# Performance work log

Hardware: AMD Instinct MI355X
Metric: run time of the kernel (lower is better)

Reference implementation:

```python
import jax, jax.numpy as jnp
import numpy as np

NV, NE, NH, NI = 50000, 10000, 512, 300000

def setup_inputs() -> dict:
    key = jax.random.key(0)
    ks = jax.random.split(key, 12)
    v = jax.random.normal(ks[0], (NV, NH), dtype=jnp.float32)
    e = jax.random.normal(ks[1], (NE, NH), dtype=jnp.float32)
    player_idx = jax.random.randint(ks[2], (NI,), 0, NV)
    game_idx = jax.random.randint(ks[3], (NI,), 0, NE)
    idx = jnp.arange(NI)
    W_v2e = jax.random.normal(ks[4], (NH, NH), dtype=jnp.float32)
    W_e2v = jax.random.normal(ks[5], (NH, NH), dtype=jnp.float32)
    b_v = jnp.zeros((NH,), dtype=jnp.float32)
    b_e = jnp.zeros((NH,), dtype=jnp.float32)
    v_weight = jax.random.uniform(ks[6], (NV, 1), dtype=jnp.float32) * 0.5 + 0.5
    e_weight = jax.random.uniform(ks[7], (NE, 1), dtype=jnp.float32) * 0.5 + 0.5
    v_reg_weight = jax.random.uniform(ks[8], (NI, 1), dtype=jnp.float32) * 0.5 + 0.5
    e_reg_weight = jax.random.uniform(ks[9], (NI, 1), dtype=jnp.float32) * 0.5 + 0.5
    e_reg_sum = jax.random.uniform(ks[10], (NE, 1), dtype=jnp.float32) + 1.0
    v_reg_sum = jax.random.uniform(ks[11], (NV, 1), dtype=jnp.float32) + 1.0
    return {"v": v, "e": e, "player_idx": player_idx, "game_idx": game_idx, "idx": idx,
            "W_v2e": W_v2e, "W_e2v": W_e2v, "b_v": b_v, "b_e": b_e,
            "v_weight": v_weight, "e_weight": e_weight,
            "v_reg_weight": v_reg_weight, "e_reg_weight": e_reg_weight,
            "v_reg_sum": v_reg_sum, "e_reg_sum": e_reg_sum}

def reference(v, e, player_idx, game_idx, idx, W_v2e, W_e2v, b_v, b_e,
              v_weight, e_weight, v_reg_weight, e_reg_weight, v_reg_sum, e_reg_sum):
    # vertex -> edge message (edge_linear=False branch: ReLU)
    ve = jax.nn.relu(v @ W_v2e + b_v)                    # [nv, nh]
    v_out = v * v_weight                                  # v_fac = 1 (predict_edge=False)
    ve_g = (ve * v_weight)[player_idx] * v_reg_weight[idx]  # [ni, nh] gather + per-incidence reg
    e_out = e + jax.ops.segment_sum(ve_g, game_idx, num_segments=NE)
    e_out = e_out / e_reg_sum
    # edge -> vertex message
    ev = jax.nn.relu(e_out @ W_e2v + b_e)                 # [ne, nh]
    ev_g = (ev * e_weight)[game_idx] * e_reg_weight[idx]  # [ni, nh]
    v_out = v_out + jax.ops.segment_sum(ev_g, player_idx, num_segments=NV)
    v_out = v_out / v_reg_sum
    # dropout_p = 0 -> identity; is_last=False, use_edge_lin=False
    return (v_out, e_out)
```

## Files before the change

kernel.cpp:

```cpp
#include <hip/hip_runtime.h>

#define NV 50000
#define NE 10000
#define NH 512
#define NI_TOT 300000
#define PB 40000

typedef __attribute__((ext_vector_type(8))) short short8v;
typedef __attribute__((ext_vector_type(4))) float f32x4;
typedef __attribute__((ext_vector_type(4))) unsigned short ushort4v;

__device__ __forceinline__ unsigned short f2bf(float x) {
    union { float f; unsigned int u; } v; v.f = x;
    unsigned int r = (v.u + 0x7FFFu + ((v.u >> 16) & 1u)) >> 16;
    return (unsigned short)r;
}
__device__ __forceinline__ unsigned int pack2bf(float lo, float hi) {
    return (unsigned int)f2bf(lo) | ((unsigned int)f2bf(hi) << 16);
}
__device__ __forceinline__ float bf2f(unsigned short u) {
    union { unsigned int x; float f; } v; v.x = ((unsigned int)u) << 16;
    return v.f;
}

__global__ __launch_bounds__(256) void cast_f32_bf16(
    const float* __restrict__ src, unsigned short* __restrict__ dst, int n8)
{
    const int i = blockIdx.x * 256 + threadIdx.x;
    if (i >= n8) return;
    const float4 a = reinterpret_cast<const float4*>(src)[2 * i];
    const float4 b = reinterpret_cast<const float4*>(src)[2 * i + 1];
    uint4 o;
    o.x = pack2bf(a.x, a.y); o.y = pack2bf(a.z, a.w);
    o.z = pack2bf(b.x, b.y); o.w = pack2bf(b.z, b.w);
    reinterpret_cast<uint4*>(dst)[i] = o;
}

__global__ __launch_bounds__(256) void gemm_mfma_bf16a_bf16out(
    const unsigned short* __restrict__ Abf, const unsigned short* __restrict__ Bt,
    const float* __restrict__ bias, const float* __restrict__ rowscale,
    unsigned short* __restrict__ Cbf, int M)
{
    __shared__ unsigned short As[128][72];
    __shared__ unsigned short Bs[128][72];

    const int tid  = threadIdx.x;
    const int lane = tid & 63;
    const int wave = tid >> 6;
    const int wm   = (wave & 1) * 64;
    const int wn   = (wave >> 1) * 64;
    const int tileM = blockIdx.y * 128;
    const int col0  = blockIdx.x * 128;

    f32x4 acc[4][4] = {};
    const short8v zero8 = {0, 0, 0, 0, 0, 0, 0, 0};

    for (int k0 = 0; k0 < NH; k0 += 64) {
        #pragma unroll
        for (int j = 0; j < 4; ++j) {
            const int chunk = j * 256 + tid;
            const int n  = chunk >> 3;
            const int kc = (chunk & 7) * 8;
            const int arow = tileM + n;
            short8v a = zero8;
            if (arow < M)
                a = *reinterpret_cast<const short8v*>(&Abf[(size_t)arow * NH + k0 + kc]);
            *reinterpret_cast<short8v*>(&As[n][kc]) = a;
        }
        #pragma unroll
        for (int j = 0; j < 4; ++j) {
            const int chunk = j * 256 + tid;
            const int n  = chunk >> 3;
            const int kc = (chunk & 7) * 8;
            short8v b = *reinterpret_cast<const short8v*>(
                &Bt[(size_t)(col0 + n) * NH + k0 + kc]);
            *reinterpret_cast<short8v*>(&Bs[n][kc]) = b;
        }
        __syncthreads();

        #pragma unroll
        for (int ks = 0; ks < 2; ++ks) {
            const int koff = ks * 32 + (lane >> 4) * 8;
            short8v af[4], bfr[4];
            #pragma unroll
            for (int mf = 0; mf < 4; ++mf)
                af[mf] = *reinterpret_cast<short8v*>(&As[wm + mf * 16 + (lane & 15)][koff]);
            #pragma unroll
            for (int nf = 0; nf < 4; ++nf)
                bfr[nf] = *reinterpret_cast<short8v*>(&Bs[wn + nf * 16 + (lane & 15)][koff]);
            #pragma unroll
            for (int mf = 0; mf < 4; ++mf)
                #pragma unroll
                for (int nf = 0; nf < 4; ++nf)
                    acc[mf][nf] = __builtin_amdgcn_mfma_f32_16x16x32_bf16(
                        af[mf], bfr[nf], acc[mf][nf], 0, 0, 0);
        }
        __syncthreads();
    }

    const int rgrp = (lane >> 4) * 4;
    const int cin  = lane & 15;
    #pragma unroll
    for (int mf = 0; mf < 4; ++mf) {
        #pragma unroll
        for (int r = 0; r < 4; ++r) {
            const int row = tileM + wm + mf * 16 + rgrp + r;
            if (row < M) {
                const float rs = rowscale[row];
                #pragma unroll
                for (int nf = 0; nf < 4; ++nf) {
                    const int col = col0 + wn + nf * 16 + cin;
                    Cbf[(size_t)row * NH + col] =
                        f2bf(fmaxf(acc[mf][nf][r] + bias[col], 0.f) * rs);
                }
            }
        }
    }
}

__global__ __launch_bounds__(256) void gemm_mfma_bf16a(
    const unsigned short* __restrict__ Abf, const unsigned short* __restrict__ Bt,
    const float* __restrict__ bias, const float* __restrict__ rowscale,
    float* __restrict__ C, int M)
{
    __shared__ unsigned short As[128][72];
    __shared__ unsigned short Bs[128][72];

    const int tid  = threadIdx.x;
    const int lane = tid & 63;
    const int wave = tid >> 6;
    const int wm   = (wave & 1) * 64;
    const int wn   = (wave >> 1) * 64;
    const int tileM = blockIdx.y * 128;
    const int col0  = blockIdx.x * 128;

    f32x4 acc[4][4] = {};
    const short8v zero8 = {0, 0, 0, 0, 0, 0, 0, 0};

    for (int k0 = 0; k0 < NH; k0 += 64) {
        #pragma unroll
        for (int j = 0; j < 4; ++j) {
            const int chunk = j * 256 + tid;
            const int n  = chunk >> 3;
            const int kc = (chunk & 7) * 8;
            const int arow = tileM + n;
            short8v a = zero8;
            if (arow < M)
                a = *reinterpret_cast<const short8v*>(&Abf[(size_t)arow * NH + k0 + kc]);
            *reinterpret_cast<short8v*>(&As[n][kc]) = a;
        }
        #pragma unroll
        for (int j = 0; j < 4; ++j) {
            const int chunk = j * 256 + tid;
            const int n  = chunk >> 3;
            const int kc = (chunk & 7) * 8;
            short8v b = *reinterpret_cast<const short8v*>(
                &Bt[(size_t)(col0 + n) * NH + k0 + kc]);
            *reinterpret_cast<short8v*>(&Bs[n][kc]) = b;
        }
        __syncthreads();

        #pragma unroll
        for (int ks = 0; ks < 2; ++ks) {
            const int koff = ks * 32 + (lane >> 4) * 8;
            short8v af[4], bfr[4];
            #pragma unroll
            for (int mf = 0; mf < 4; ++mf)
                af[mf] = *reinterpret_cast<short8v*>(&As[wm + mf * 16 + (lane & 15)][koff]);
            #pragma unroll
            for (int nf = 0; nf < 4; ++nf)
                bfr[nf] = *reinterpret_cast<short8v*>(&Bs[wn + nf * 16 + (lane & 15)][koff]);
            #pragma unroll
            for (int mf = 0; mf < 4; ++mf)
                #pragma unroll
                for (int nf = 0; nf < 4; ++nf)
                    acc[mf][nf] = __builtin_amdgcn_mfma_f32_16x16x32_bf16(
                        af[mf], bfr[nf], acc[mf][nf], 0, 0, 0);
        }
        __syncthreads();
    }

    const int rgrp = (lane >> 4) * 4;
    const int cin  = lane & 15;
    #pragma unroll
    for (int mf = 0; mf < 4; ++mf) {
        #pragma unroll
        for (int r = 0; r < 4; ++r) {
            const int row = tileM + wm + mf * 16 + rgrp + r;
            if (row < M) {
                const float rs = rowscale[row];
                #pragma unroll
                for (int nf = 0; nf < 4; ++nf) {
                    const int col = col0 + wn + nf * 16 + cin;
                    C[(size_t)row * NH + col] = fmaxf(acc[mf][nf][r] + bias[col], 0.f) * rs;
                }
            }
        }
    }
}

__global__ __launch_bounds__(256) void gemm_mfma_relu_scale(
    const float* __restrict__ A, const unsigned short* __restrict__ Bt,
    const float* __restrict__ bias, const float* __restrict__ rowscale,
    float* __restrict__ C, int M)
{
    __shared__ unsigned short As[128][72];
    __shared__ unsigned short Bs[128][72];

    const int tid  = threadIdx.x;
    const int lane = tid & 63;
    const int wave = tid >> 6;
    const int wm   = (wave & 1) * 64;
    const int wn   = (wave >> 1) * 64;
    const int tileM = blockIdx.y * 128;
    const int col0  = blockIdx.x * 128;

    f32x4 acc[4][4] = {};

    for (int k0 = 0; k0 < NH; k0 += 64) {
        #pragma unroll
        for (int j = 0; j < 8; ++j) {
            const int r = j * 16 + (tid >> 4);
            const int c = (tid & 15) * 4;
            const int arow = tileM + r;
            float4 av = make_float4(0.f, 0.f, 0.f, 0.f);
            if (arow < M)
                av = *reinterpret_cast<const float4*>(&A[(size_t)arow * NH + k0 + c]);
            unsigned short* dst = &As[r][c];
            dst[0] = f2bf(av.x); dst[1] = f2bf(av.y);
            dst[2] = f2bf(av.z); dst[3] = f2bf(av.w);
        }
        #pragma unroll
        for (int j = 0; j < 4; ++j) {
            const int chunk = j * 256 + tid;
            const int n  = chunk >> 3;
            const int kc = (chunk & 7) * 8;
            short8v b = *reinterpret_cast<const short8v*>(
                &Bt[(size_t)(col0 + n) * NH + k0 + kc]);
            *reinterpret_cast<short8v*>(&Bs[n][kc]) = b;
        }
        __syncthreads();

        #pragma unroll
        for (int ks = 0; ks < 2; ++ks) {
            const int koff = ks * 32 + (lane >> 4) * 8;
            short8v af[4], bfr[4];
            #pragma unroll
            for (int mf = 0; mf < 4; ++mf)
                af[mf] = *reinterpret_cast<short8v*>(&As[wm + mf * 16 + (lane & 15)][koff]);
            #pragma unroll
            for (int nf = 0; nf < 4; ++nf)
                bfr[nf] = *reinterpret_cast<short8v*>(&Bs[wn + nf * 16 + (lane & 15)][koff]);
            #pragma unroll
            for (int mf = 0; mf < 4; ++mf)
                #pragma unroll
                for (int nf = 0; nf < 4; ++nf)
                    acc[mf][nf] = __builtin_amdgcn_mfma_f32_16x16x32_bf16(
                        af[mf], bfr[nf], acc[mf][nf], 0, 0, 0);
        }
        __syncthreads();
    }

    const int rgrp = (lane >> 4) * 4;
    const int cin  = lane & 15;
    #pragma unroll
    for (int mf = 0; mf < 4; ++mf) {
        #pragma unroll
        for (int r = 0; r < 4; ++r) {
            const int row = tileM + wm + mf * 16 + rgrp + r;
            if (row < M) {
                const float rs = rowscale[row];
                #pragma unroll
                for (int nf = 0; nf < 4; ++nf) {
                    const int col = col0 + wn + nf * 16 + cin;
                    C[(size_t)row * NH + col] = fmaxf(acc[mf][nf][r] + bias[col], 0.f) * rs;
                }
            }
        }
    }
}

__global__ __launch_bounds__(256) void transpose_cast_w(
    const float* __restrict__ W, unsigned short* __restrict__ Wt)
{
    __shared__ float t[32][33];
    const int bx = blockIdx.x;
    const int by = blockIdx.y;
    const int tx = threadIdx.x & 31;
    const int ty = threadIdx.x >> 5;
    #pragma unroll
    for (int j = 0; j < 32; j += 8)
        t[ty + j][tx] = W[(size_t)(by * 32 + ty + j) * NH + bx * 32 + tx];
    __syncthreads();
    #pragma unroll
    for (int j = 0; j < 32; j += 8)
        Wt[(size_t)(bx * 32 + ty + j) * NH + by * 32 + tx] = f2bf(t[tx][ty + j]);
}

__global__ __launch_bounds__(256) void gemm_relu_scale(
    const float* __restrict__ A, const float* __restrict__ B,
    const float* __restrict__ bias, const float* __restrict__ rowscale,
    float* __restrict__ C, int M)
{
    __shared__ float As[16][68];
    __shared__ float Bs[16][64];
    const int tid = threadIdx.x;
    const int tx = tid & 15;
    const int ty = tid >> 4;
    const int tileM = blockIdx.y * 64;
    const int col0  = blockIdx.x * 64;
    const int lr  = tid >> 2;
    const int lk4 = (tid & 3) * 4;
    const int bc  = tid & 63;
    const int bk  = tid >> 6;
    float acc[4][4] = {};
    for (int k0 = 0; k0 < NH; k0 += 16) {
        const int arow = tileM + lr;
        float4 av = make_float4(0.f, 0.f, 0.f, 0.f);
        if (arow < M)
            av = *reinterpret_cast<const float4*>(&A[(size_t)arow * NH + k0 + lk4]);
        As[lk4 + 0][lr] = av.x; As[lk4 + 1][lr] = av.y;
        As[lk4 + 2][lr] = av.z; As[lk4 + 3][lr] = av.w;
        #pragma unroll
        for (int jj = 0; jj < 4; ++jj) {
            const int kk = bk + jj * 4;
            Bs[kk][bc] = B[(size_t)(k0 + kk) * NH + col0 + bc];
        }
        __syncthreads();
        #pragma unroll
        for (int kk = 0; kk < 16; ++kk) {
            float4 a = *reinterpret_cast<const float4*>(&As[kk][ty * 4]);
            float4 b = *reinterpret_cast<const float4*>(&Bs[kk][tx * 4]);
            acc[0][0] += a.x * b.x; acc[0][1] += a.x * b.y; acc[0][2] += a.x * b.z; acc[0][3] += a.x * b.w;
            acc[1][0] += a.y * b.x; acc[1][1] += a.y * b.y; acc[1][2] += a.y * b.z; acc[1][3] += a.y * b.w;
            acc[2][0] += a.z * b.x; acc[2][1] += a.z * b.y; acc[2][2] += a.z * b.z; acc[2][3] += a.z * b.w;
            acc[3][0] += a.w * b.x; acc[3][1] += a.w * b.y; acc[3][2] += a.w * b.z; acc[3][3] += a.w * b.w;
        }
        __syncthreads();
    }
    const int rbase = tileM + ty * 4;
    const int cbase = col0 + tx * 4;
    #pragma unroll
    for (int i = 0; i < 4; ++i) {
        const int row = rbase + i;
        if (row < M) {
            const float s = rowscale[row];
            float4 o;
            o.x = fmaxf(acc[i][0] + bias[cbase + 0], 0.f) * s;
            o.y = fmaxf(acc[i][1] + bias[cbase + 1], 0.f) * s;
            o.z = fmaxf(acc[i][2] + bias[cbase + 2], 0.f) * s;
            o.w = fmaxf(acc[i][3] + bias[cbase + 3], 0.f) * s;
            *reinterpret_cast<float4*>(&C[(size_t)row * NH + cbase]) = o;
        }
    }
}

__global__ __launch_bounds__(256) void zero_ints(int* __restrict__ p, int n)
{
    const int i = blockIdx.x * 256 + threadIdx.x;
    if (i < n) p[i] = 0;
}

__global__ __launch_bounds__(256) void hist_kernel(
    const int* __restrict__ gi, const int* __restrict__ pi,
    int* __restrict__ e_cnt, int* __restrict__ v_cnt)
{
    const int i = blockIdx.x * 256 + threadIdx.x;
    if (i >= NI_TOT) return;
    atomicAdd(&e_cnt[gi[i]], 1);
    atomicAdd(&v_cnt[pi[i]], 1);
}

__global__ __launch_bounds__(256) void scan_local(
    const int* __restrict__ cnt, int* __restrict__ off, int* __restrict__ bsum, int n)
{
    __shared__ int buf[256];
    const int t = threadIdx.x;
    const int gi = blockIdx.x * 256 + t;
    int x = (gi < n) ? cnt[gi] : 0;
    buf[t] = x;
    __syncthreads();
    #pragma unroll
    for (int d = 1; d < 256; d <<= 1) {
        int y = (t >= d) ? buf[t - d] : 0;
        __syncthreads();
        buf[t] += y;
        __syncthreads();
    }
    if (gi < n) off[gi + 1] = buf[t];
    if (t == 255) bsum[blockIdx.x] = buf[255];
}

__global__ __launch_bounds__(256) void scan_bsums(int* __restrict__ bsum, int nb)
{
    __shared__ int buf[256];
    const int t = threadIdx.x;
    const int x = (t < nb) ? bsum[t] : 0;
    buf[t] = x;
    __syncthreads();
    #pragma unroll
    for (int d = 1; d < 256; d <<= 1) {
        int y = (t >= d) ? buf[t - d] : 0;
        __syncthreads();
        buf[t] += y;
        __syncthreads();
    }
    if (t < nb) bsum[t] = buf[t] - x;
}

__global__ __launch_bounds__(256) void scan_add(
    int* __restrict__ off, const int* __restrict__ bsum, int n)
{
    const int gi = blockIdx.x * 256 + threadIdx.x;
    if (gi == 0) off[0] = 0;
    if (gi < n) off[gi + 1] += bsum[blockIdx.x];
}

__global__ __launch_bounds__(256) void scan_kernel(
    const int* __restrict__ cnt, int* __restrict__ off, int n)
{
    __shared__ int buf[256];
    __shared__ int carry_s;
    const int t = threadIdx.x;
    if (t == 0) { off[0] = 0; carry_s = 0; }
    __syncthreads();
    for (int base = 0; base < n; base += 256) {
        int x = (base + t < n) ? cnt[base + t] : 0;
        buf[t] = x;
        __syncthreads();
        #pragma unroll
        for (int d = 1; d < 256; d <<= 1) {
            int y = (t >= d) ? buf[t - d] : 0;
            __syncthreads();
            buf[t] += y;
            __syncthreads();
        }
        if (base + t < n) off[base + t + 1] = buf[t] + carry_s;
        __syncthreads();
        if (t == 255) carry_s += buf[255];
        __syncthreads();
    }
}

__global__ __launch_bounds__(256) void fill_kernel(
    const int* __restrict__ gi, const int* __restrict__ pi,
    const int* __restrict__ e_off, int* __restrict__ e_cur, int* __restrict__ e_list,
    const int* __restrict__ v_off, int* __restrict__ v_cur, int* __restrict__ v_list)
{
    const int i = blockIdx.x * 256 + threadIdx.x;
    if (i >= NI_TOT) return;
    const int g = gi[i];
    e_list[e_off[g] + atomicAdd(&e_cur[g], 1)] = i;
    const int p = pi[i];
    v_list[v_off[p] + atomicAdd(&v_cur[p], 1)] = i;
}

__global__ __launch_bounds__(128) void agg_e_bf16(
    const float* __restrict__ e, const unsigned short* __restrict__ ve_bf,
    const int* __restrict__ player_idx, const float* __restrict__ v_reg_weight,
    const int* __restrict__ e_off, const int* __restrict__ e_list,
    const float* __restrict__ e_reg_sum, float* __restrict__ out_e,
    unsigned short* __restrict__ Ebf)
{
    __shared__ int   sp[128];
    __shared__ float sw[128];
    const int g = blockIdx.x;
    const int t = threadIdx.x;
    const int c = t << 2;
    float4 acc = *reinterpret_cast<const float4*>(&e[(size_t)g * NH + c]);
    const int beg = e_off[g], end = e_off[g + 1];
    for (int base = beg; base < end; base += 128) {
        const int m = min(128, end - base);
        __syncthreads();
        if (t < m) {
            const int i = e_list[base + t];
            sp[t] = player_idx[i];
            sw[t] = v_reg_weight[i];
        }
        __syncthreads();
        #pragma unroll 4
        for (int j = 0; j < m; ++j) {
            const int   p = sp[j];
            const float w = sw[j];
            ushort4v x = *reinterpret_cast<const ushort4v*>(&ve_bf[(size_t)p * NH + c]);
            acc.x += w * bf2f(x.x); acc.y += w * bf2f(x.y);
            acc.z += w * bf2f(x.z); acc.w += w * bf2f(x.w);
        }
    }
    const float inv = 1.0f / e_reg_sum[g];
    acc.x *= inv; acc.y *= inv; acc.z *= inv; acc.w *= inv;
    *reinterpret_cast<float4*>(&out_e[(size_t)g * NH + c]) = acc;
    uint2 pk;
    pk.x = pack2bf(acc.x, acc.y);
    pk.y = pack2bf(acc.z, acc.w);
    *reinterpret_cast<uint2*>(&Ebf[(size_t)g * NH + c]) = pk;
}

__global__ __launch_bounds__(128) void agg_v_bf16(
    const float* __restrict__ v, const float* __restrict__ v_weight,
    const unsigned short* __restrict__ ev_bf,
    const int* __restrict__ game_idx, const float* __restrict__ e_reg_weight,
    const int* __restrict__ v_off, const int* __restrict__ v_list,
    const float* __restrict__ v_reg_sum, float* __restrict__ out_v)
{
    __shared__ int   sg[128];
    __shared__ float sw[128];
    const int p = blockIdx.x;
    const int t = threadIdx.x;
    const int c = t << 2;
    const float vw = v_weight[p];
    float4 acc = *reinterpret_cast<const float4*>(&v[(size_t)p * NH + c]);
    acc.x *= vw; acc.y *= vw; acc.z *= vw; acc.w *= vw;
    const int beg = v_off[p], end = v_off[p + 1];
    for (int base = beg; base < end; base += 128) {
        const int m = min(128, end - base);
        __syncthreads();
        if (t < m) {
            const int i = v_list[base + t];
            sg[t] = game_idx[i];
            sw[t] = e_reg_weight[i];
        }
        __syncthreads();
        #pragma unroll 4
        for (int j = 0; j < m; ++j) {
            const int   g = sg[j];
            const float w = sw[j];
            ushort4v x = *reinterpret_cast<const ushort4v*>(&ev_bf[(size_t)g * NH + c]);
            acc.x += w * bf2f(x.x); acc.y += w * bf2f(x.y);
            acc.z += w * bf2f(x.z); acc.w += w * bf2f(x.w);
        }
    }
    const float inv = 1.0f / v_reg_sum[p];
    acc.x *= inv; acc.y *= inv; acc.z *= inv; acc.w *= inv;
    *reinterpret_cast<float4*>(&out_v[(size_t)p * NH + c]) = acc;
}

__global__ __launch_bounds__(128) void agg_e_kernel(
    const float* __restrict__ e, const float* __restrict__ ve_w,
    const int* __restrict__ player_idx, const float* __restrict__ v_reg_weight,
    const int* __restrict__ e_off, const int* __restrict__ e_list,
    const float* __restrict__ e_reg_sum, float* __restrict__ out_e)
{
    __shared__ int   sp[128];
    __shared__ float sw[128];
    const int g = blockIdx.x;
    const int t = threadIdx.x;
    const int c = t << 2;
    float4 acc = *reinterpret_cast<const float4*>(&e[(size_t)g * NH + c]);
    const int beg = e_off[g], end = e_off[g + 1];
    for (int base = beg; base < end; base += 128) {
        const int m = min(128, end - base);
        __syncthreads();
        if (t < m) {
            const int i = e_list[base + t];
            sp[t] = player_idx[i];
            sw[t] = v_reg_weight[i];
        }
        __syncthreads();
        #pragma unroll 4
        for (int j = 0; j < m; ++j) {
            const int   p = sp[j];
            const float w = sw[j];
            float4 x = *reinterpret_cast<const float4*>(&ve_w[(size_t)p * NH + c]);
            acc.x += w * x.x; acc.y += w * x.y; acc.z += w * x.z; acc.w += w * x.w;
        }
    }
    const float inv = 1.0f / e_reg_sum[g];
    acc.x *= inv; acc.y *= inv; acc.z *= inv; acc.w *= inv;
    *reinterpret_cast<float4*>(&out_e[(size_t)g * NH + c]) = acc;
}

__global__ __launch_bounds__(128) void agg_v_kernel(
    const float* __restrict__ v, const float* __restrict__ v_weight,
    const float* __restrict__ ev_w,
    const int* __restrict__ game_idx, const float* __restrict__ e_reg_weight,
    const int* __restrict__ v_off, const int* __restrict__ v_list,
    const float* __restrict__ v_reg_sum, float* __restrict__ out_v)
{
    __shared__ int   sg[128];
    __shared__ float sw[128];
    const int p = blockIdx.x;
    const int t = threadIdx.x;
    const int c = t << 2;
    const float vw = v_weight[p];
    float4 acc = *reinterpret_cast<const float4*>(&v[(size_t)p * NH + c]);
    acc.x *= vw; acc.y *= vw; acc.z *= vw; acc.w *= vw;
    const int beg = v_off[p], end = v_off[p + 1];
    for (int base = beg; base < end; base += 128) {
        const int m = min(128, end - base);
        __syncthreads();
        if (t < m) {
            const int i = v_list[base + t];
            sg[t] = game_idx[i];
            sw[t] = e_reg_weight[i];
        }
        __syncthreads();
        #pragma unroll 4
        for (int j = 0; j < m; ++j) {
            const int   g = sg[j];
            const float w = sw[j];
            float4 x = *reinterpret_cast<const float4*>(&ev_w[(size_t)g * NH + c]);
            acc.x += w * x.x; acc.y += w * x.y; acc.z += w * x.z; acc.w += w * x.w;
        }
    }
    const float inv = 1.0f / v_reg_sum[p];
    acc.x *= inv; acc.y *= inv; acc.z *= inv; acc.w *= inv;
    *reinterpret_cast<float4*>(&out_v[(size_t)p * NH + c]) = acc;
}

__global__ __launch_bounds__(256) void scatter_add_kernel(
    const float* __restrict__ src, const int* __restrict__ gidx,
    const int* __restrict__ sidx, const float* __restrict__ regw,
    float* __restrict__ dst, int ni, int smin, int smax, int gmax)
{
    const int i = blockIdx.x * 2 + (threadIdx.x >> 7);
    if (i >= ni) return;
    const int s = sidx[i];
    if (s < smin || s >= smax) return;
    const int g = gidx[i];
    if (g < 0 || g >= gmax) return;
    const int c = (threadIdx.x & 127) << 2;
    const float w = regw[i];
    float4 val = *reinterpret_cast<const float4*>(&src[(size_t)g * NH + c]);
    float* d = &dst[(size_t)s * NH + c];
    atomicAdd(d + 0, val.x * w);
    atomicAdd(d + 1, val.y * w);
    atomicAdd(d + 2, val.z * w);
    atomicAdd(d + 3, val.w * w);
}

__global__ __launch_bounds__(256) void recompute_ev_scatter(
    const float* __restrict__ e_out, const float* __restrict__ W,
    const float* __restrict__ bias, const float* __restrict__ e_weight,
    const int* __restrict__ player_idx, const int* __restrict__ game_idx,
    const float* __restrict__ e_reg_weight, float* __restrict__ out_v, int pmin)
{
    const int i = blockIdx.x;
    const int p = player_idx[i];
    if (p < pmin || p >= NV) return;
    const int g = game_idx[i];
    if (g < 0 || g >= NE) return;
    __shared__ float eg[NH];
    const int t = threadIdx.x;
    eg[t]       = e_out[(size_t)g * NH + t];
    eg[t + 256] = e_out[(size_t)g * NH + t + 256];
    __syncthreads();
    float s0 = 0.f, s1 = 0.f;
    #pragma unroll 4
    for (int k = 0; k < NH; ++k) {
        const float ek = eg[k];
        s0 += ek * W[(size_t)k * NH + t];
        s1 += ek * W[(size_t)k * NH + t + 256];
    }
    const float ew = e_weight[g] * e_reg_weight[i];
    atomicAdd(&out_v[(size_t)p * NH + t],       fmaxf(s0 + bias[t], 0.f) * ew);
    atomicAdd(&out_v[(size_t)p * NH + t + 256], fmaxf(s1 + bias[t + 256], 0.f) * ew);
}

__global__ __launch_bounds__(256) void init_copy(
    const float* __restrict__ src, float* __restrict__ dst, int n4)
{
    const int i = blockIdx.x * 256 + threadIdx.x;
    if (i < n4)
        reinterpret_cast<float4*>(dst)[i] = reinterpret_cast<const float4*>(src)[i];
}

__global__ __launch_bounds__(256) void init_scale_rows(
    const float* __restrict__ src, const float* __restrict__ w,
    float* __restrict__ dst, int n4)
{
    const int i = blockIdx.x * 256 + threadIdx.x;
    if (i >= n4) return;
    const int row = i >> 7;
    const float s = w[row];
    float4 v = reinterpret_cast<const float4*>(src)[i];
    v.x *= s; v.y *= s; v.z *= s; v.w *= s;
    reinterpret_cast<float4*>(dst)[i] = v;
}

__global__ __launch_bounds__(256) void div_rows(
    const float* __restrict__ rs, float* __restrict__ x, int n4)
{
    const int i = blockIdx.x * 256 + threadIdx.x;
    if (i >= n4) return;
    const int row = i >> 7;
    const float inv = 1.0f / rs[row];
    float4 v = reinterpret_cast<float4*>(x)[i];
    v.x *= inv; v.y *= inv; v.z *= inv; v.w *= inv;
    reinterpret_cast<float4*>(x)[i] = v;
}

extern "C" void kernel_launch(void* const* d_in, const int* in_sizes, int n_in,
                              void* d_out, int out_size, void* d_ws, size_t ws_size,
                              hipStream_t stream) {
    const float* v            = (const float*)d_in[0];
    const float* e            = (const float*)d_in[1];
    const int*   player_idx   = (const int*)d_in[2];
    const int*   game_idx     = (const int*)d_in[3];
    const float* W_v2e        = (const float*)d_in[5];
    const float* W_e2v        = (const float*)d_in[6];
    const float* b_v          = (const float*)d_in[7];
    const float* b_e          = (const float*)d_in[8];

    const float* a9  = (const float*)d_in[9];
    const float* a10 = (const float*)d_in[10];
    const float* v_weight = (in_sizes[9]  == NV) ? a9  : a10;
    const float* e_weight = (in_sizes[9]  == NV) ? a10 : a9;
    const float* v_reg_weight = (const float*)d_in[11];
    const float* e_reg_weight = (const float*)d_in[12];
    const float* a13 = (const float*)d_in[13];
    const float* a14 = (const float*)d_in[14];
    const float* e_reg_sum = (in_sizes[13] == NE) ? a13 : a14;
    const float* v_reg_sum = (in_sizes[13] == NE) ? a14 : a13;

    float* out_v = (float*)d_out;
    float* out_e = (float*)d_out + (size_t)NV * NH;

    const dim3 blk(256);
    const int NB_E = (NE + 255) / 256;
    const int NB_V = (NV + 255) / 256;

    float* ev_w = (float*)d_ws;
    int* e_cnt  = (int*)((char*)d_ws + (size_t)NE * NH * sizeof(float));
    int* v_cnt  = e_cnt + NE;
    int* e_cur  = v_cnt + NV;
    int* v_cur  = e_cur + NE;
    int* e_off  = v_cur + NV;
    int* v_off  = e_off + NE + 1;
    int* e_list = v_off + NV + 1;
    int* v_list = e_list + NI_TOT;
    int* e_bsum = v_list + NI_TOT;
    int* v_bsum = e_bsum + NB_E;
    unsigned short* Wt1 = (unsigned short*)(v_bsum + NB_V);
    unsigned short* Wt2 = Wt1 + (size_t)NH * NH;
    unsigned short* Abf = Wt2 + (size_t)NH * NH;
    unsigned short* Ebf = Abf + (size_t)NV * NH;
    const size_t csr_need  = (size_t)((char*)(v_list + NI_TOT) - (char*)d_ws);
    const size_t mfma_need = (size_t)((char*)(Abf)            - (char*)d_ws);
    const size_t bf16_need = (size_t)((char*)(Ebf + (size_t)NE * NH) - (char*)d_ws);

    if (ws_size >= mfma_need && d_ws != nullptr) {
        const bool bf16a = (ws_size >= bf16_need);
        transpose_cast_w<<<dim3(16, 16), blk, 0, stream>>>(W_v2e, Wt1);
        transpose_cast_w<<<dim3(16, 16), blk, 0, stream>>>(W_e2v, Wt2);
        if (bf16a)
            cast_f32_bf16<<<(NV * NH / 8 + 255) / 256, blk, 0, stream>>>(
                v, Abf, NV * NH / 8);
        const int nz = 2 * (NE + NV);
        zero_ints<<<(nz + 255) / 256, blk, 0, stream>>>(e_cnt, nz);
        hist_kernel<<<(NI_TOT + 255) / 256, blk, 0, stream>>>(
            game_idx, player_idx, e_cnt, v_cnt);
        scan_local<<<NB_E, blk, 0, stream>>>(e_cnt, e_off, e_bsum, NE);
        scan_bsums<<<1, blk, 0, stream>>>(e_bsum, NB_E);
        scan_add<<<NB_E, blk, 0, stream>>>(e_off, e_bsum, NE);
        scan_local<<<NB_V, blk, 0, stream>>>(v_cnt, v_off, v_bsum, NV);
        scan_bsums<<<1, blk, 0, stream>>>(v_bsum, NB_V);
        scan_add<<<NB_V, blk, 0, stream>>>(v_off, v_bsum, NV);
        fill_kernel<<<(NI_TOT + 255) / 256, blk, 0, stream>>>(
            game_idx, player_idx, e_off, e_cur, e_list, v_off, v_cur, v_list);

        if (bf16a) {
            unsigned short* ve_bf = (unsigned short*)out_v;
            gemm_mfma_bf16a_bf16out<<<dim3(NH / 128, (NV + 127) / 128), blk, 0, stream>>>(
                Abf, Wt1, b_v, v_weight, ve_bf, NV);
            agg_e_bf16<<<NE, dim3(128), 0, stream>>>(
                e, ve_bf, player_idx, v_reg_weight, e_off, e_list, e_reg_sum,
                out_e, Ebf);
            unsigned short* ev_bf = (unsigned short*)ev_w;
            gemm_mfma_bf16a_bf16out<<<dim3(NH / 128, (NE + 127) / 128), blk, 0, stream>>>(
                Ebf, Wt2, b_e, e_weight, ev_bf, NE);
            agg_v_bf16<<<NV, dim3(128), 0, stream>>>(
                v, v_weight, ev_bf, game_idx, e_reg_weight, v_off, v_list,
                v_reg_sum, out_v);
        } else {
            gemm_mfma_relu_scale<<<dim3(NH / 128, (NV + 127) / 128), blk, 0, stream>>>(
                v, Wt1, b_v, v_weight, out_v, NV);
            agg_e_kernel<<<NE, dim3(128), 0, stream>>>(
                e, out_v, player_idx, v_reg_weight, e_off, e_list, e_reg_sum, out_e);
            gemm_mfma_relu_scale<<<dim3(NH / 128, (NE + 127) / 128), blk, 0, stream>>>(
                out_e, Wt2, b_e, e_weight, ev_w, NE);
            agg_v_kernel<<<NV, dim3(128), 0, stream>>>(
                v, v_weight, ev_w, game_idx, e_reg_weight, v_off, v_list,
                v_reg_sum, out_v);
        }
        return;
    }

    if (ws_size >= csr_need && d_ws != nullptr) {
        gemm_relu_scale<<<dim3(NH / 64, (NV + 63) / 64), blk, 0, stream>>>(
            v, W_v2e, b_v, v_weight, out_v, NV);
        const int nz = 2 * (NE + NV);
        zero_ints<<<(nz + 255) / 256, blk, 0, stream>>>(e_cnt, nz);
        hist_kernel<<<(NI_TOT + 255) / 256, blk, 0, stream>>>(
            game_idx, player_idx, e_cnt, v_cnt);
        scan_kernel<<<1, blk, 0, stream>>>(e_cnt, e_off, NE);
        scan_kernel<<<1, blk, 0, stream>>>(v_cnt, v_off, NV);
        fill_kernel<<<(NI_TOT + 255) / 256, blk, 0, stream>>>(
            game_idx, player_idx, e_off, e_cur, e_list, v_off, v_cur, v_list);
        agg_e_kernel<<<NE, dim3(128), 0, stream>>>(
            e, out_v, player_idx, v_reg_weight, e_off, e_list, e_reg_sum, out_e);
        gemm_relu_scale<<<dim3(NH / 64, (NE + 63) / 64), blk, 0, stream>>>(
            out_e, W_e2v, b_e, e_weight, ev_w, NE);
        agg_v_kernel<<<NV, dim3(128), 0, stream>>>(
            v, v_weight, ev_w, game_idx, e_reg_weight, v_off, v_list,
            v_reg_sum, out_v);
        return;
    }

    const size_t evw_bytes = (size_t)NE * NH * sizeof(float);
    const bool big_ws = (ws_size >= evw_bytes) && (d_ws != nullptr);
    float* ev_w2 = big_ws ? (float*)d_ws : (out_v + (size_t)PB * NH);
    const int pb = big_ws ? NV : PB;
    const int n4_e = NE * NH / 4;

    gemm_relu_scale<<<dim3(NH / 64, (NV + 63) / 64), blk, 0, stream>>>(
        v, W_v2e, b_v, v_weight, out_v, NV);
    init_copy<<<(n4_e + 255) / 256, blk, 0, stream>>>(e, out_e, n4_e);
    scatter_add_kernel<<<(NI_TOT + 1) / 2, blk, 0, stream>>>(
        out_v, player_idx, game_idx, v_reg_weight, out_e, NI_TOT, 0, NE, NV);
    div_rows<<<(n4_e + 255) / 256, blk, 0, stream>>>(e_reg_sum, out_e, n4_e);
    gemm_relu_scale<<<dim3(NH / 64, (NE + 63) / 64), blk, 0, stream>>>(
        out_e, W_e2v, b_e, e_weight, ev_w2, NE);
    {
        const int n4 = pb * NH / 4;
        init_scale_rows<<<(n4 + 255) / 256, blk, 0, stream>>>(v, v_weight, out_v, n4);
    }
    scatter_add_kernel<<<(NI_TOT + 1) / 2, blk, 0, stream>>>(
        ev_w2, game_idx, player_idx, e_reg_weight, out_v, NI_TOT, 0, pb, NE);
    {
        const int n4 = pb * NH / 4;
        div_rows<<<(n4 + 255) / 256, blk, 0, stream>>>(v_reg_sum, out_v, n4);
    }
    if (!big_ws) {
        const int n4t = (NV - PB) * NH / 4;
        init_scale_rows<<<(n4t + 255) / 256, blk, 0, stream>>>(
            v + (size_t)PB * NH, v_weight + PB, out_v + (size_t)PB * NH, n4t);
        recompute_ev_scatter<<<NI_TOT, blk, 0, stream>>>(
            out_e, W_e2v, b_e, e_weight, player_idx, game_idx, e_reg_weight,
            out_v, PB);
        div_rows<<<(n4t + 255) / 256, blk, 0, stream>>>(
            v_reg_sum + PB, out_v + (size_t)PB * NH, n4t);
    }
}
```

Measured before the change: 340.8 us.

## Pre-tile and swizzle bf16 operands and load GEMM tiles via direct global-to-LDS

```diff
diff --git a/kernel.cpp b/kernel.cpp
--- a/kernel.cpp
+++ b/kernel.cpp
@@ -5,6 +5,7 @@
 #define NH 512
 #define NI_TOT 300000
 #define PB 40000
+#define NT_A 391
 
 typedef __attribute__((ext_vector_type(8))) short short8v;
 typedef __attribute__((ext_vector_type(4))) float f32x4;
@@ -22,18 +23,148 @@
     union { unsigned int x; float f; } v; v.x = ((unsigned int)u) << 16;
     return v.f;
 }
-
-__global__ __launch_bounds__(256) void cast_f32_bf16(
-    const float* __restrict__ src, unsigned short* __restrict__ dst, int n8)
+__device__ __forceinline__ void gload16(const void* g, void* l) {
+    __builtin_amdgcn_global_load_lds(
+        (const __attribute__((address_space(1))) unsigned int*)g,
+        (__attribute__((address_space(3))) unsigned int*)l, 16, 0, 0);
+}
+
+__global__ __launch_bounds__(256) void cast_tile_swz(
+    const float* __restrict__ src, unsigned short* __restrict__ dst,
+    int M, int ngroups)
 {
     const int i = blockIdx.x * 256 + threadIdx.x;
-    if (i >= n8) return;
-    const float4 a = reinterpret_cast<const float4*>(src)[2 * i];
-    const float4 b = reinterpret_cast<const float4*>(src)[2 * i + 1];
-    uint4 o;
-    o.x = pack2bf(a.x, a.y); o.y = pack2bf(a.z, a.w);
-    o.z = pack2bf(b.x, b.y); o.w = pack2bf(b.z, b.w);
-    reinterpret_cast<uint4*>(dst)[i] = o;
+    if (i >= ngroups) return;
+    const int r  = i >> 6;
+    const int gq = i & 63;
+    uint4 o = make_uint4(0u, 0u, 0u, 0u);
+    if (r < M) {
+        const float4 a = *reinterpret_cast<const float4*>(&src[(size_t)r * NH + gq * 8]);
+        const float4 b = *reinterpret_cast<const float4*>(&src[(size_t)r * NH + gq * 8 + 4]);
+        o.x = pack2bf(a.x, a.y); o.y = pack2bf(a.z, a.w);
+        o.z = pack2bf(b.x, b.y); o.w = pack2bf(b.z, b.w);
+    }
+    const size_t base = ((size_t)(r >> 7) * 8 + (gq >> 3)) * 16384;
+    const int phys = (((r & 127) * 128 + (gq & 7) * 16)) ^ ((r & 7) << 4);
+    *reinterpret_cast<uint4*>((char*)dst + base + phys) = o;
+}
+
+__global__ __launch_bounds__(256) void transpose_cast_w_tiled(
+    const float* __restrict__ W, unsigned short* __restrict__ Wt)
+{
+    __shared__ float t[32][33];
+    const int bx = blockIdx.x;
+    const int by = blockIdx.y;
+    const int tx = threadIdx.x & 31;
+    const int ty = threadIdx.x >> 5;
+    #pragma unroll
+    for (int j = 0; j < 32; j += 8)
+        t[ty + j][tx] = W[(size_t)(by * 32 + ty + j) * NH + bx * 32 + tx];
+    __syncthreads();
+    #pragma unroll
+    for (int j = 0; j < 32; j += 8) {
+        const int n = bx * 32 + ty + j;
+        const int k = by * 32 + tx;
+        const size_t base = ((size_t)(n >> 7) * 8 + (k >> 6)) * 16384;
+        const int phys = (((n & 127) * 128 + (k & 63) * 2)) ^ ((n & 7) << 4);
+        *reinterpret_cast<unsigned short*>((char*)Wt + base + phys) = f2bf(t[tx][ty + j]);
+    }
+}
+
+__global__ __launch_bounds__(256) void transpose_cast_w(
+    const float* __restrict__ W, unsigned short* __restrict__ Wt)
+{
+    __shared__ float t[32][33];
+    const int bx = blockIdx.x;
+    const int by = blockIdx.y;
+    const int tx = threadIdx.x & 31;
+    const int ty = threadIdx.x >> 5;
+    #pragma unroll
+    for (int j = 0; j < 32; j += 8)
+        t[ty + j][tx] = W[(size_t)(by * 32 + ty + j) * NH + bx * 32 + tx];
+    __syncthreads();
+    #pragma unroll
+    for (int j = 0; j < 32; j += 8)
+        Wt[(size_t)(bx * 32 + ty + j) * NH + by * 32 + tx] = f2bf(t[tx][ty + j]);
+}
+
+__global__ __launch_bounds__(256) void gemm_mfma_gld(
+    const unsigned short* __restrict__ At, const unsigned short* __restrict__ Btl,
+    const float* __restrict__ bias, const float* __restrict__ rowscale,
+    unsigned short* __restrict__ Cbf, int M)
+{
+    __shared__ __align__(16) unsigned char As[16384];
+    __shared__ __align__(16) unsigned char Bs[16384];
+
+    const int tid  = threadIdx.x;
+    const int lane = tid & 63;
+    const int wave = tid >> 6;
+    const int wm   = (wave & 1) * 64;
+    const int wn   = (wave >> 1) * 64;
+    const int tileM = blockIdx.y * 128;
+    const int col0  = blockIdx.x * 128;
+
+    const char* Abase = (const char*)At  + (size_t)blockIdx.y * 8 * 16384;
+    const char* Bbase = (const char*)Btl + (size_t)blockIdx.x * 8 * 16384;
+
+    f32x4 acc[4][4] = {};
+
+    for (int s = 0; s < 8; ++s) {
+        const char* ga = Abase + s * 16384 + (size_t)wave * 4096 + lane * 16;
+        const char* gb = Bbase + s * 16384 + (size_t)wave * 4096 + lane * 16;
+        char* la = (char*)As + wave * 4096;
+        char* lb = (char*)Bs + wave * 4096;
+        #pragma unroll
+        for (int i = 0; i < 4; ++i) {
+            gload16(ga + i * 1024, la + i * 1024);
+            gload16(gb + i * 1024, lb + i * 1024);
+        }
+        __syncthreads();
+
+        #pragma unroll
+        for (int ks = 0; ks < 2; ++ks) {
+            const int kb = ks * 64 + (lane >> 4) * 16;
+            short8v af[4], bfr[4];
+            #pragma unroll
+            for (int mf = 0; mf < 4; ++mf) {
+                const int r = wm + mf * 16 + (lane & 15);
+                af[mf] = *reinterpret_cast<const short8v*>(
+                    (const char*)As + ((r * 128 + kb) ^ ((r & 7) << 4)));
+            }
+            #pragma unroll
+            for (int nf = 0; nf < 4; ++nf) {
+                const int n = wn + nf * 16 + (lane & 15);
+                bfr[nf] = *reinterpret_cast<const short8v*>(
+                    (const char*)Bs + ((n * 128 + kb) ^ ((n & 7) << 4)));
+            }
+            #pragma unroll
+            for (int mf = 0; mf < 4; ++mf)
+                #pragma unroll
+                for (int nf = 0; nf < 4; ++nf)
+                    acc[mf][nf] = __builtin_amdgcn_mfma_f32_16x16x32_bf16(
+                        af[mf], bfr[nf], acc[mf][nf], 0, 0, 0);
+        }
+        __syncthreads();
+    }
+
+    const int rgrp = (lane >> 4) * 4;
+    const int cin  = lane & 15;
+    #pragma unroll
+    for (int mf = 0; mf < 4; ++mf) {
+        #pragma unroll
+        for (int r = 0; r < 4; ++r) {
+            const int row = tileM + wm + mf * 16 + rgrp + r;
+            if (row < M) {
+                const float rs = rowscale[row];
+                #pragma unroll
+                for (int nf = 0; nf < 4; ++nf) {
+                    const int col = col0 + wn + nf * 16 + cin;
+                    Cbf[(size_t)row * NH + col] =
+                        f2bf(fmaxf(acc[mf][nf][r] + bias[col], 0.f) * rs);
+                }
+            }
+        }
+    }
 }
 
 __global__ __launch_bounds__(256) void gemm_mfma_bf16a_bf16out(
@@ -116,185 +247,6 @@
             }
         }
     }
-}
-
-__global__ __launch_bounds__(256) void gemm_mfma_bf16a(
-    const unsigned short* __restrict__ Abf, const unsigned short* __restrict__ Bt,
-    const float* __restrict__ bias, const float* __restrict__ rowscale,
-    float* __restrict__ C, int M)
-{
-    __shared__ unsigned short As[128][72];
-    __shared__ unsigned short Bs[128][72];
-
-    const int tid  = threadIdx.x;
-    const int lane = tid & 63;
-    const int wave = tid >> 6;
-    const int wm   = (wave & 1) * 64;
-    const int wn   = (wave >> 1) * 64;
-    const int tileM = blockIdx.y * 128;
-    const int col0  = blockIdx.x * 128;
-
-    f32x4 acc[4][4] = {};
-    const short8v zero8 = {0, 0, 0, 0, 0, 0, 0, 0};
-
-    for (int k0 = 0; k0 < NH; k0 += 64) {
-        #pragma unroll
-        for (int j = 0; j < 4; ++j) {
-            const int chunk = j * 256 + tid;
-            const int n  = chunk >> 3;
-            const int kc = (chunk & 7) * 8;
-            const int arow = tileM + n;
-            short8v a = zero8;
-            if (arow < M)
-                a = *reinterpret_cast<const short8v*>(&Abf[(size_t)arow * NH + k0 + kc]);
-            *reinterpret_cast<short8v*>(&As[n][kc]) = a;
-        }
-        #pragma unroll
-        for (int j = 0; j < 4; ++j) {
-            const int chunk = j * 256 + tid;
-            const int n  = chunk >> 3;
-            const int kc = (chunk & 7) * 8;
-            short8v b = *reinterpret_cast<const short8v*>(
-                &Bt[(size_t)(col0 + n) * NH + k0 + kc]);
-            *reinterpret_cast<short8v*>(&Bs[n][kc]) = b;
-        }
-        __syncthreads();
-
-        #pragma unroll
-        for (int ks = 0; ks < 2; ++ks) {
-            const int koff = ks * 32 + (lane >> 4) * 8;
-            short8v af[4], bfr[4];
-            #pragma unroll
-            for (int mf = 0; mf < 4; ++mf)
-                af[mf] = *reinterpret_cast<short8v*>(&As[wm + mf * 16 + (lane & 15)][koff]);
-            #pragma unroll
-            for (int nf = 0; nf < 4; ++nf)
-                bfr[nf] = *reinterpret_cast<short8v*>(&Bs[wn + nf * 16 + (lane & 15)][koff]);
-            #pragma unroll
-            for (int mf = 0; mf < 4; ++mf)
-                #pragma unroll
-                for (int nf = 0; nf < 4; ++nf)
-                    acc[mf][nf] = __builtin_amdgcn_mfma_f32_16x16x32_bf16(
-                        af[mf], bfr[nf], acc[mf][nf], 0, 0, 0);
-        }
-        __syncthreads();
-    }
-
-    const int rgrp = (lane >> 4) * 4;
-    const int cin  = lane & 15;
-    #pragma unroll
-    for (int mf = 0; mf < 4; ++mf) {
-        #pragma unroll
-        for (int r = 0; r < 4; ++r) {
-            const int row = tileM + wm + mf * 16 + rgrp + r;
-            if (row < M) {
-                const float rs = rowscale[row];
-                #pragma unroll
-                for (int nf = 0; nf < 4; ++nf) {
-                    const int col = col0 + wn + nf * 16 + cin;
-                    C[(size_t)row * NH + col] = fmaxf(acc[mf][nf][r] + bias[col], 0.f) * rs;
-                }
-            }
-        }
-    }
-}
-
-__global__ __launch_bounds__(256) void gemm_mfma_relu_scale(
-    const float* __restrict__ A, const unsigned short* __restrict__ Bt,
-    const float* __restrict__ bias, const float* __restrict__ rowscale,
-    float* __restrict__ C, int M)
-{
-    __shared__ unsigned short As[128][72];
-    __shared__ unsigned short Bs[128][72];
-
-    const int tid  = threadIdx.x;
-    const int lane = tid & 63;
-    const int wave = tid >> 6;
-    const int wm   = (wave & 1) * 64;
-    const int wn   = (wave >> 1) * 64;
-    const int tileM = blockIdx.y * 128;
-    const int col0  = blockIdx.x * 128;
-
-    f32x4 acc[4][4] = {};
-
-    for (int k0 = 0; k0 < NH; k0 += 64) {
-        #pragma unroll
-        for (int j = 0; j < 8; ++j) {
-            const int r = j * 16 + (tid >> 4);
-            const int c = (tid & 15) * 4;
-            const int arow = tileM + r;
-            float4 av = make_float4(0.f, 0.f, 0.f, 0.f);
-            if (arow < M)
-                av = *reinterpret_cast<const float4*>(&A[(size_t)arow * NH + k0 + c]);
-            unsigned short* dst = &As[r][c];
-            dst[0] = f2bf(av.x); dst[1] = f2bf(av.y);
-            dst[2] = f2bf(av.z); dst[3] = f2bf(av.w);
-        }
-        #pragma unroll
-        for (int j = 0; j < 4; ++j) {
-            const int chunk = j * 256 + tid;
-            const int n  = chunk >> 3;
-            const int kc = (chunk & 7) * 8;
-            short8v b = *reinterpret_cast<const short8v*>(
-                &Bt[(size_t)(col0 + n) * NH + k0 + kc]);
-            *reinterpret_cast<short8v*>(&Bs[n][kc]) = b;
-        }
-        __syncthreads();
-
-        #pragma unroll
-        for (int ks = 0; ks < 2; ++ks) {
-            const int koff = ks * 32 + (lane >> 4) * 8;
-            short8v af[4], bfr[4];
-            #pragma unroll
-            for (int mf = 0; mf < 4; ++mf)
-                af[mf] = *reinterpret_cast<short8v*>(&As[wm + mf * 16 + (lane & 15)][koff]);
-            #pragma unroll
-            for (int nf = 0; nf < 4; ++nf)
-                bfr[nf] = *reinterpret_cast<short8v*>(&Bs[wn + nf * 16 + (lane & 15)][koff]);
-            #pragma unroll
-            for (int mf = 0; mf < 4; ++mf)
-                #pragma unroll
-                for (int nf = 0; nf < 4; ++nf)
-                    acc[mf][nf] = __builtin_amdgcn_mfma_f32_16x16x32_bf16(
-                        af[mf], bfr[nf], acc[mf][nf], 0, 0, 0);
-        }
-        __syncthreads();
-    }
-
-    const int rgrp = (lane >> 4) * 4;
-    const int cin  = lane & 15;
-    #pragma unroll
-    for (int mf = 0; mf < 4; ++mf) {
-        #pragma unroll
-        for (int r = 0; r < 4; ++r) {
-            const int row = tileM + wm + mf * 16 + rgrp + r;
-            if (row < M) {
-                const float rs = rowscale[row];
-                #pragma unroll
-                for (int nf = 0; nf < 4; ++nf) {
-                    const int col = col0 + wn + nf * 16 + cin;
-                    C[(size_t)row * NH + col] = fmaxf(acc[mf][nf][r] + bias[col], 0.f) * rs;
-                }
-            }
-        }
-    }
-}
-
-__global__ __launch_bounds__(256) void transpose_cast_w(
-    const float* __restrict__ W, unsigned short* __restrict__ Wt)
-{
-    __shared__ float t[32][33];
-    const int bx = blockIdx.x;
-    const int by = blockIdx.y;
-    const int tx = threadIdx.x & 31;
-    const int ty = threadIdx.x >> 5;
-    #pragma unroll
-    for (int j = 0; j < 32; j += 8)
-        t[ty + j][tx] = W[(size_t)(by * 32 + ty + j) * NH + bx * 32 + tx];
-    __syncthreads();
-    #pragma unroll
-    for (int j = 0; j < 32; j += 8)
-        Wt[(size_t)(bx * 32 + ty + j) * NH + by * 32 + tx] = f2bf(t[tx][ty + j]);
 }
 
 __global__ __launch_bounds__(256) void gemm_relu_scale(
@@ -720,8 +672,9 @@
     const int NB_E = (NE + 255) / 256;
     const int NB_V = (NV + 255) / 256;
 
-    float* ev_w = (float*)d_ws;
-    int* e_cnt  = (int*)((char*)d_ws + (size_t)NE * NH * sizeof(float));
+    unsigned short* ev_bf = (unsigned short*)d_ws;
+    unsigned short* Ebf   = ev_bf + (size_t)NE * NH;
+    int* e_cnt  = (int*)(Ebf + (size_t)NE * NH);
     int* v_cnt  = e_cnt + NE;
     int* e_cur  = v_cnt + NV;
     int* v_cur  = e_cur + NE;
@@ -731,21 +684,16 @@
     int* v_list = e_list + NI_TOT;
     int* e_bsum = v_list + NI_TOT;
     int* v_bsum = e_bsum + NB_E;
-    unsigned short* Wt1 = (unsigned short*)(v_bsum + NB_V);
-    unsigned short* Wt2 = Wt1 + (size_t)NH * NH;
-    unsigned short* Abf = Wt2 + (size_t)NH * NH;
-    unsigned short* Ebf = Abf + (size_t)NV * NH;
-    const size_t csr_need  = (size_t)((char*)(v_list + NI_TOT) - (char*)d_ws);
-    const size_t mfma_need = (size_t)((char*)(Abf)            - (char*)d_ws);
-    const size_t bf16_need = (size_t)((char*)(Ebf + (size_t)NE * NH) - (char*)d_ws);
-
-    if (ws_size >= mfma_need && d_ws != nullptr) {
-        const bool bf16a = (ws_size >= bf16_need);
-        transpose_cast_w<<<dim3(16, 16), blk, 0, stream>>>(W_v2e, Wt1);
+    unsigned short* Wt1t = (unsigned short*)(v_bsum + NB_V);
+    unsigned short* Wt2  = Wt1t + (size_t)4 * 8 * 8192;
+    unsigned short* Abft = Wt2 + (size_t)NH * NH;
+    const size_t fast_need = (size_t)((char*)(Abft + (size_t)NT_A * 8 * 8192) - (char*)d_ws);
+
+    if (ws_size >= fast_need && d_ws != nullptr) {
+        transpose_cast_w_tiled<<<dim3(16, 16), blk, 0, stream>>>(W_v2e, Wt1t);
         transpose_cast_w<<<dim3(16, 16), blk, 0, stream>>>(W_e2v, Wt2);
-        if (bf16a)
-            cast_f32_bf16<<<(NV * NH / 8 + 255) / 256, blk, 0, stream>>>(
-                v, Abf, NV * NH / 8);
+        const int ngroups = NT_A * 128 * 64;
+        cast_tile_swz<<<(ngroups + 255) / 256, blk, 0, stream>>>(v, Abft, NV, ngroups);
         const int nz = 2 * (NE + NV);
         zero_ints<<<(nz + 255) / 256, blk, 0, stream>>>(e_cnt, nz);
         hist_kernel<<<(NI_TOT + 255) / 256, blk, 0, stream>>>(
@@ -758,51 +706,48 @@
         scan_add<<<NB_V, blk, 0, stream>>>(v_off, v_bsum, NV);
         fill_kernel<<<(NI_TOT + 255) / 256, blk, 0, stream>>>(
             game_idx, player_idx, e_off, e_cur, e_list, v_off, v_cur, v_list);
-
-        if (bf16a) {
-            unsigned short* ve_bf = (unsigned short*)out_v;
-            gemm_mfma_bf16a_bf16out<<<dim3(NH / 128, (NV + 127) / 128), blk, 0, stream>>>(
-                Abf, Wt1, b_v, v_weight, ve_bf, NV);
-            agg_e_bf16<<<NE, dim3(128), 0, stream>>>(
-                e, ve_bf, player_idx, v_reg_weight, e_off, e_list, e_reg_sum,
-                out_e, Ebf);
-            unsigned short* ev_bf = (unsigned short*)ev_w;
-            gemm_mfma_bf16a_bf16out<<<dim3(NH / 128, (NE + 127) / 128), blk, 0, stream>>>(
-                Ebf, Wt2, b_e, e_weight, ev_bf, NE);
-            agg_v_bf16<<<NV, dim3(128), 0, stream>>>(
-                v, v_weight, ev_bf, game_idx, e_reg_weight, v_off, v_list,
-                v_reg_sum, out_v);
-        } else {
-            gemm_mfma_relu_scale<<<dim3(NH / 128, (NV + 127) / 128), blk, 0, stream>>>(
-                v, Wt1, b_v, v_weight, out_v, NV);
-            agg_e_kernel<<<NE, dim3(128), 0, stream>>>(
-                e, out_v, player_idx, v_reg_weight, e_off, e_list, e_reg_sum, out_e);
-            gemm_mfma_relu_scale<<<dim3(NH / 128, (NE + 127) / 128), blk, 0, stream>>>(
-                out_e, Wt2, b_e, e_weight, ev_w, NE);
-            agg_v_kernel<<<NV, dim3(128), 0, stream>>>(
-                v, v_weight, ev_w, game_idx, e_reg_weight, v_off, v_list,
-                v_reg_sum, out_v);
-        }
+        unsigned short* ve_bf = (unsigned short*)out_v;
+        gemm_mfma_gld<<<dim3(NH / 128, NT_A), blk, 0, stream>>>(
+            Abft, Wt1t, b_v, v_weight, ve_bf, NV);
+        agg_e_bf16<<<NE, dim3(128), 0, stream>>>(
+            e, ve_bf, player_idx, v_reg_weight, e_off, e_list, e_reg_sum,
+            out_e, Ebf);
+        gemm_mfma_bf16a_bf16out<<<dim3(NH / 128, (NE + 127) / 128), blk, 0, stream>>>(
+            Ebf, Wt2, b_e, e_weight, ev_bf, NE);
+        agg_v_bf16<<<NV, dim3(128), 0, stream>>>(
+            v, v_weight, ev_bf, game_idx, e_reg_weight, v_off, v_list,
+            v_reg_sum, out_v);
         return;
     }
+
+    float* ev_w = (float*)d_ws;
+    int* f_e_cnt  = (int*)((char*)d_ws + (size_t)NE * NH * sizeof(float));
+    int* f_v_cnt  = f_e_cnt + NE;
+    int* f_e_cur  = f_v_cnt + NV;
+    int* f_v_cur  = f_e_cur + NE;
+    int* f_e_off  = f_v_cur + NV;
+    int* f_v_off  = f_e_off + NE + 1;
+    int* f_e_list = f_v_off + NV + 1;
+    int* f_v_list = f_e_list + NI_TOT;
+    const size_t csr_need = (size_t)((char*)(f_v_list + NI_TOT) - (char*)d_ws);
 
     if (ws_size >= csr_need && d_ws != nullptr) {
         gemm_relu_scale<<<dim3(NH / 64, (NV + 63) / 64), blk, 0, stream>>>(
             v, W_v2e, b_v, v_weight, out_v, NV);
         const int nz = 2 * (NE + NV);
-        zero_ints<<<(nz + 255) / 256, blk, 0, stream>>>(e_cnt, nz);
+        zero_ints<<<(nz + 255) / 256, blk, 0, stream>>>(f_e_cnt, nz);
         hist_kernel<<<(NI_TOT + 255) / 256, blk, 0, stream>>>(
-            game_idx, player_idx, e_cnt, v_cnt);
-        scan_kernel<<<1, blk, 0, stream>>>(e_cnt, e_off, NE);
-        scan_kernel<<<1, blk, 0, stream>>>(v_cnt, v_off, NV);
+            game_idx, player_idx, f_e_cnt, f_v_cnt);
+        scan_kernel<<<1, blk, 0, stream>>>(f_e_cnt, f_e_off, NE);
+        scan_kernel<<<1, blk, 0, stream>>>(f_v_cnt, f_v_off, NV);
         fill_kernel<<<(NI_TOT + 255) / 256, blk, 0, stream>>>(
-            game_idx, player_idx, e_off, e_cur, e_list, v_off, v_cur, v_list);
+            game_idx, player_idx, f_e_off, f_e_cur, f_e_list, f_v_off, f_v_cur, f_v_list);
         agg_e_kernel<<<NE, dim3(128), 0, stream>>>(
-            e, out_v, player_idx, v_reg_weight, e_off, e_list, e_reg_sum, out_e);
+            e, out_v, player_idx, v_reg_weight, f_e_off, f_e_list, e_reg_sum, out_e);
         gemm_relu_scale<<<dim3(NH / 64, (NE + 63) / 64), blk, 0, stream>>>(
             out_e, W_e2v, b_e, e_weight, ev_w, NE);
         agg_v_kernel<<<NV, dim3(128), 0, stream>>>(
-            v, v_weight, ev_w, game_idx, e_reg_weight, v_off, v_list,
+            v, v_weight, ev_w, game_idx, e_reg_weight, f_v_off, f_v_list,
             v_reg_sum, out_v);
         return;
     }
```

Measured after the change: 326.0 us. -4.3%, faster.
